# Performance work log

Hardware: AMD Instinct MI355X
Metric: run time of the kernel (lower is better)

## Reference

```python
import jax, jax.numpy as jnp
import numpy as np

B, C, D, H, K = 512, 112, 128, 8, 8  # batch, channels(=seq), d_model, heads, conv kernel
HD = D // H
SCALE = HD ** -0.5
BN_EPS = 1e-5
LN_EPS = 1e-5


def setup_inputs() -> dict:
    key = jax.random.key(0)
    ks = jax.random.split(key, 12)
    s = 0.05
    return {
        "x": jax.random.normal(ks[0], (B, C, D), jnp.float32),
        "conv_w": jax.random.normal(ks[1], (C, 1, K), jnp.float32) * s,
        "conv_b": jax.random.normal(ks[2], (C,), jnp.float32) * s,
        "bn_g": jnp.ones((C,), jnp.float32),
        "bn_b": jnp.zeros((C,), jnp.float32),
        "bn_m": jnp.zeros((C,), jnp.float32),
        "bn_v": jnp.ones((C,), jnp.float32),
        "wq": jax.random.normal(ks[3], (D, D), jnp.float32) * s,
        "bq": jax.random.normal(ks[4], (D,), jnp.float32) * s,
        "wk": jax.random.normal(ks[5], (D, D), jnp.float32) * s,
        "bk": jax.random.normal(ks[6], (D,), jnp.float32) * s,
        "wv": jax.random.normal(ks[7], (D, D), jnp.float32) * s,
        "bv": jax.random.normal(ks[8], (D,), jnp.float32) * s,
        "wo": jax.random.normal(ks[9], (D, D), jnp.float32) * s,
        "bo": jax.random.normal(ks[10], (D,), jnp.float32) * s,
        "ln_g": jnp.ones((D,), jnp.float32),
        "ln_b": jnp.zeros((D,), jnp.float32),
    }


def _forward(x, conv_w, conv_b, bn_g, bn_b, bn_m, bn_v,
             wq, bq, wk, bk, wv, bv, wo, bo, ln_g, ln_b):
    # resnet_1: depthwise Conv1d(padding='same', k=8) -> GELU -> BatchNorm1d (eval)
    # torch 'same' padding for even k: left = (k-1)//2 = 3, right = 4
    h = jax.lax.conv_general_dilated(
        x, conv_w, window_strides=(1,), padding=[(3, 4)],
        dimension_numbers=("NCH", "OIH", "NCH"), feature_group_count=C)
    h = h + conv_b[None, :, None]
    h = jax.nn.gelu(h, approximate=False)
    h = (h - bn_m[None, :, None]) * (bn_g[None, :, None] * jax.lax.rsqrt(bn_v + BN_EPS)[None, :, None]) + bn_b[None, :, None]
    src = x + h  # [B, C, D]; attention treats C as sequence dim

    # multi-head attention (hand-rolled, res_attention path with prev=None)
    q = (src @ wq.T + bq).reshape(B, C, H, HD).transpose(0, 2, 1, 3)  # [B,H,S,hd]
    k = (src @ wk.T + bk).reshape(B, C, H, HD).transpose(0, 2, 1, 3)
    v = (src @ wv.T + bv).reshape(B, C, H, HD).transpose(0, 2, 1, 3)
    scores = jnp.einsum("bhqd,bhkd->bhqk", q, k) * SCALE  # [B,H,S,S]
    attn = jax.nn.softmax(scores, axis=-1)
    out = jnp.einsum("bhqk,bhkd->bhqd", attn, v)  # [B,H,S,hd]
    out = out.transpose(0, 2, 1, 3).reshape(B, C, D)
    out = out @ wo.T + bo

    # residual + LayerNorm over last dim
    src = src + out
    mu = jnp.mean(src, axis=-1, keepdims=True)
    var = jnp.mean(jnp.square(src - mu), axis=-1, keepdims=True)
    src = (src - mu) * jax.lax.rsqrt(var + LN_EPS) * ln_g + ln_b
    return src


def reference(x, conv_w, conv_b, bn_g, bn_b, bn_m, bn_v,
              wq, bq, wk, bk, wv, bv, wo, bo, ln_g, ln_b):
    return _forward(x, conv_w, conv_b, bn_g, bn_b, bn_m, bn_v,
                    wq, bq, wk, bk, wv, bv, wo, bo, ln_g, ln_b)
```

## Files before the change

kernel.cpp:

```cpp
#include <hip/hip_runtime.h>
#include <hip/hip_bf16.h>

#define BB 512
#define CC 112
#define DD 128
#define HH 8
#define HD 16
#define KK 8
#define SROW 140
#define QS 1792

typedef unsigned short u16;
typedef short short8 __attribute__((ext_vector_type(8)));
typedef float f32x4 __attribute__((ext_vector_type(4)));
typedef float f32x16 __attribute__((ext_vector_type(16)));

#define MFMA16(a, b, c) __builtin_amdgcn_mfma_f32_16x16x32_bf16(a, b, c, 0, 0, 0)
#define MFMA32(a, b, c) __builtin_amdgcn_mfma_f32_32x32x16_bf16(a, b, c, 0, 0, 0)

__device__ inline u16 f2bf(float f) {
  union { float f; unsigned u; } v{f};
  unsigned r = (v.u + 0x7FFFu + ((v.u >> 16) & 1u)) >> 16;
  return (u16)r;
}
__device__ inline float bf2f(u16 u) {
  union { unsigned u; float f; } v;
  v.u = ((unsigned)u) << 16;
  return v.f;
}
__device__ inline unsigned pk2(float a, float b) {
  __hip_bfloat162 h = __float22bfloat162_rn(float2{a, b});
  union { __hip_bfloat162 h; unsigned u; } v{h};
  return v.u;
}

__device__ inline unsigned permx32(unsigned x) {
  unsigned a = x, b = x;
  asm("v_permlane32_swap_b32 %0, %1" : "+v"(a), "+v"(b));
  return (threadIdx.x & 32) ? a : b;
}
__device__ inline float permx32f(float x) {
  union { float f; unsigned u; } v{x};
  v.u = permx32(v.u);
  return v.f;
}

__global__ __launch_bounds__(256) void k_wcvt(
    const float* __restrict__ wq, const float* __restrict__ wk,
    const float* __restrict__ wv, const float* __restrict__ wo,
    u16* __restrict__ w_b) {
  const int i = (blockIdx.x * 256 + threadIdx.x);
  const int sel = i >> 12, off = i & 4095;
  const float* w = (sel == 0) ? wq : (sel == 1) ? wk : (sel == 2) ? wv : wo;
  const float4 v = ((const float4*)w)[off];
  ((uint2*)w_b)[i] = uint2{pk2(v.x, v.y), pk2(v.z, v.w)};
}

__global__ __launch_bounds__(1024, 4) void k_fused(
    const float* __restrict__ x, const float* __restrict__ cw,
    const float* __restrict__ cb, const float* __restrict__ bg,
    const float* __restrict__ bb_, const float* __restrict__ bm,
    const float* __restrict__ bv, const u16* __restrict__ w_b,
    const float* __restrict__ bq, const float* __restrict__ bk,
    const float* __restrict__ bvv, const float* __restrict__ bo,
    const float* __restrict__ lg, const float* __restrict__ lb,
    float* __restrict__ out) {
  __shared__ __attribute__((aligned(16))) u16 S[CC * SROW];
  __shared__ __attribute__((aligned(16))) u16 QL[HH * CC * HD];
  __shared__ __attribute__((aligned(16))) u16 KL[HH * CC * HD];
  __shared__ __attribute__((aligned(16))) u16 VTL[HH * HD * CC];
  const int b = blockIdx.x;
  const int t = threadIdx.x;
  const int wave = t >> 6, lane = t & 63;

  const int tg = t >> 3, s = t & 7;
  if (tg < CC) {
    const int row = tg, ch = tg;
    const float4 w0 = *(const float4*)(cw + ch * KK);
    const float4 w1 = *(const float4*)(cw + ch * KK + 4);
    const float cbv = cb[ch];
    const float bscale = bg[ch] * rsqrtf(bv[ch] + 1e-5f);
    const float bmv = bm[ch], bbv = bb_[ch];
    const float* __restrict__ xr = x + ((size_t)b * CC + row) * DD;
    float in[24];
#pragma unroll
    for (int f = 0; f < 6; ++f) {
      const int fi = 4 * s - 1 + f;
      float4 vv = {0.f, 0.f, 0.f, 0.f};
      if (fi >= 0 && fi < 32) vv = ((const float4*)xr)[fi];
      in[f * 4 + 0] = vv.x; in[f * 4 + 1] = vv.y;
      in[f * 4 + 2] = vv.z; in[f * 4 + 3] = vv.w;
    }
    unsigned pkv[8];
#pragma unroll
    for (int i2 = 0; i2 < 8; ++i2) {
      float oo[2];
#pragma unroll
      for (int j = 0; j < 2; ++j) {
        const int i = i2 * 2 + j;
        float a = 0.f;
        a = fmaf(in[i + 1], w0.x, a);
        a = fmaf(in[i + 2], w0.y, a);
        a = fmaf(in[i + 3], w0.z, a);
        a = fmaf(in[i + 4], w0.w, a);
        a = fmaf(in[i + 5], w1.x, a);
        a = fmaf(in[i + 6], w1.y, a);
        a = fmaf(in[i + 7], w1.z, a);
        a = fmaf(in[i + 8], w1.w, a);
        a += cbv;
        const float u = fmaf(0.044715f * a, a, 1.0f);
        const float e = __expf(a * u * -1.5957691216f);
        const float g = a * __frcp_rn(1.f + e);
        oo[j] = in[i + 4] + (g - bmv) * bscale + bbv;
      }
      pkv[i2] = pk2(oo[0], oo[1]);
    }
    u16* srow = S + row * SROW + s * 16;
#pragma unroll
    for (int k2 = 0; k2 < 4; ++k2)
      *(uint2*)(srow + k2 * 4) = ((uint2*)pkv)[k2];
  }
  __syncthreads();

  {
    const int h = wave >> 1, mh = wave & 1;
    const int quad = lane >> 4, n = lane & 15;
    short8 Bf0[4], Bf1[4], Bf2[4];
#pragma unroll
    for (int kf = 0; kf < 4; ++kf) {
      const int wi = (h * 16 + n) * DD + kf * 32 + quad * 8;
      Bf0[kf] = *(const short8*)(w_b + wi);
      Bf1[kf] = *(const short8*)(w_b + 16384 + wi);
      Bf2[kf] = *(const short8*)(w_b + 32768 + wi);
    }
    const float bqv = bq[h * 16 + n];
    const float bkv = bk[h * 16 + n];
    const float bvv2 = bvv[h * 16 + n];
    u16* qlh = QL + h * QS;
    u16* klh = KL + h * QS;
    u16* vlh = VTL + h * QS;
#pragma unroll
    for (int m = 0; m < 4; ++m) {
      const int mt = mh * 4 + m;
      if (mt < 7) {
        short8 A[4];
#pragma unroll
        for (int kf = 0; kf < 4; ++kf)
          A[kf] = *(const short8*)&S[(mt * 16 + n) * SROW + kf * 32 + quad * 8];
        f32x4 aq = {0.f, 0.f, 0.f, 0.f};
        f32x4 ak = {0.f, 0.f, 0.f, 0.f};
        f32x4 av = {0.f, 0.f, 0.f, 0.f};
#pragma unroll
        for (int kf = 0; kf < 4; ++kf) {
          aq = MFMA16(A[kf], Bf0[kf], aq);
          ak = MFMA16(A[kf], Bf1[kf], ak);
          av = MFMA16(A[kf], Bf2[kf], av);
        }
        const int row0 = mt * 16 + quad * 4;
#pragma unroll
        for (int r = 0; r < 4; ++r) {
          qlh[(row0 + r) * HD + n] = f2bf(aq[r] + bqv);
          klh[(row0 + r) * HD + n] = f2bf(ak[r] + bkv);
        }
        *(uint2*)&vlh[n * CC + row0] =
            uint2{pk2(av[0] + bvv2, av[1] + bvv2),
                  pk2(av[2] + bvv2, av[3] + bvv2)};
      }
    }
  }
  __syncthreads();

  {
    const int h = wave >> 1, qh = wave & 1;
    const int lo = lane & 31, hi = lane >> 5, hi8 = hi * 8;
    const u16* qlh = QL + h * QS;
    const u16* klh = KL + h * QS;
    const u16* vlh = VTL + h * QS;
    u16* aoh = QL + h * QS;
    for (int qi = 0; qi < 2; ++qi) {
      const int qt = qh * 2 + qi;
      const int qt0 = qt * 32;
      short8 Bq = {};
      if (qt0 + lo < CC) Bq = *(const short8*)(qlh + (qt0 + lo) * HD + hi8);
      f32x16 sa[4];
#pragma unroll
      for (int mt = 0; mt < 4; ++mt) {
        short8 Ak = {};
        const int key = mt * 32 + lo;
        if (key < CC) Ak = *(const short8*)(klh + key * HD + hi8);
        f32x16 z = {};
        sa[mt] = MFMA32(Ak, Bq, z);
      }
      const float C1 = 0.25f * 1.44269504088896341f;
      float mxp[4] = {-1e30f, -1e30f, -1e30f, -1e30f};
#pragma unroll
      for (int mt = 0; mt < 4; ++mt) {
        const int rmax = (mt == 3) ? 8 : 16;
#pragma unroll
        for (int r = 0; r < 16; ++r)
          if (r < rmax) mxp[r & 3] = fmaxf(mxp[r & 3], sa[mt][r]);
      }
      float mx = fmaxf(fmaxf(mxp[0], mxp[1]), fmaxf(mxp[2], mxp[3]));
      mx = fmaxf(mx, permx32f(mx));
      const float mxc = mx * C1;
      float sp[4] = {0.f, 0.f, 0.f, 0.f};
#pragma unroll
      for (int mt = 0; mt < 4; ++mt) {
        const int rmax = (mt == 3) ? 8 : 16;
#pragma unroll
        for (int r = 0; r < 16; ++r)
          if (r < rmax) {
            const float p = exp2f(fmaf(sa[mt][r], C1, -mxc));
            sa[mt][r] = p;
            sp[r & 3] += p;
          }
      }
      float sum = (sp[0] + sp[1]) + (sp[2] + sp[3]);
      sum += permx32f(sum);
      const float rinv = 1.f / sum;
      unsigned U0[4][4], U1[4][4];
#pragma unroll
      for (int mt = 0; mt < 4; ++mt) {
        const int rqmax = (mt == 3) ? 2 : 4;
#pragma unroll
        for (int rq = 0; rq < 4; ++rq)
          if (rq < rqmax) {
            U0[mt][rq] =
                pk2(sa[mt][4 * rq + 0] * rinv, sa[mt][4 * rq + 1] * rinv);
            U1[mt][rq] =
                pk2(sa[mt][4 * rq + 2] * rinv, sa[mt][4 * rq + 3] * rinv);
          }
      }
      f32x16 oacc = {};
#pragma unroll
      for (int kt = 0; kt < 7; ++kt) {
        const int mt = kt >> 1;
        const int c = 2 * (kt & 1);
        const unsigned own0 = hi ? U0[mt][c + 1] : U0[mt][c];
        const unsigned own1 = hi ? U1[mt][c + 1] : U1[mt][c];
        const unsigned snd0 = hi ? U0[mt][c] : U0[mt][c + 1];
        const unsigned snd1 = hi ? U1[mt][c] : U1[mt][c + 1];
        const unsigned got0 = permx32(snd0);
        const unsigned got1 = permx32(snd1);
        union { unsigned u[4]; short8 s; } ap;
        ap.u[0] = hi ? got0 : own0;
        ap.u[1] = hi ? got1 : own1;
        ap.u[2] = hi ? own0 : got0;
        ap.u[3] = hi ? own1 : got1;
        short8 Bv = {};
        if (lo < HD) Bv = *(const short8*)(vlh + lo * CC + kt * 16 + hi8);
        oacc = MFMA32(ap.s, Bv, oacc);
      }
      if (lo < HD) {
#pragma unroll
        for (int r = 0; r < 16; ++r) {
          const int rr = (r & 3) + 8 * (r >> 2) + 4 * hi;
          if (qt0 + rr < CC) aoh[(qt0 + rr) * HD + lo] = f2bf(oacc[r]);
        }
      }
    }
  }
  __syncthreads();

  if (wave < 7) {
    const int quad = lane >> 4, n = lane & 15;
    const int mt = wave;
    const u16* __restrict__ w_bo = w_b + 3 * 16384;
    short8 A[4];
#pragma unroll
    for (int kf = 0; kf < 4; ++kf) {
      const int head = 2 * kf + (quad >> 1);
      A[kf] = *(const short8*)&QL[head * QS + (mt * 16 + n) * HD + (quad & 1) * 8];
    }
    float v[8][4];
#pragma unroll
    for (int nt = 0; nt < 8; ++nt) {
      f32x4 acc = {0.f, 0.f, 0.f, 0.f};
#pragma unroll
      for (int kf = 0; kf < 4; ++kf) {
        const short8 Bf =
            *(const short8*)(w_bo + (nt * 16 + n) * DD + kf * 32 + quad * 8);
        acc = MFMA16(A[kf], Bf, acc);
      }
      const int col = nt * 16 + n;
      const float bcol = bo[col];
#pragma unroll
      for (int r = 0; r < 4; ++r)
        v[nt][r] = acc[r] + bcol +
                   bf2f(S[(mt * 16 + quad * 4 + r) * SROW + col]);
    }
    float sum[4] = {0.f, 0.f, 0.f, 0.f}, sq[4] = {0.f, 0.f, 0.f, 0.f};
#pragma unroll
    for (int nt = 0; nt < 8; ++nt)
#pragma unroll
      for (int r = 0; r < 4; ++r) {
        sum[r] += v[nt][r];
        sq[r] = fmaf(v[nt][r], v[nt][r], sq[r]);
      }
#pragma unroll
    for (int d = 1; d < 16; d <<= 1)
#pragma unroll
      for (int r = 0; r < 4; ++r) {
        sum[r] += __shfl_xor(sum[r], d);
        sq[r] += __shfl_xor(sq[r], d);
      }
    float mu[4], rs[4];
#pragma unroll
    for (int r = 0; r < 4; ++r) {
      mu[r] = sum[r] * (1.f / DD);
      const float var = sq[r] * (1.f / DD) - mu[r] * mu[r];
      rs[r] = rsqrtf(var + 1e-5f);
    }
#pragma unroll
    for (int nt = 0; nt < 8; ++nt) {
      const int col = nt * 16 + n;
      const float g = lg[col], be = lb[col];
#pragma unroll
      for (int r = 0; r < 4; ++r)
        out[((size_t)b * CC + mt * 16 + quad * 4 + r) * DD + col] =
            (v[nt][r] - mu[r]) * rs[r] * g + be;
    }
  }
}

extern "C" void kernel_launch(void* const* d_in, const int* in_sizes, int n_in,
                              void* d_out, int out_size, void* d_ws,
                              size_t ws_size, hipStream_t stream) {
  (void)in_sizes; (void)n_in; (void)out_size; (void)ws_size;
  const float* x   = (const float*)d_in[0];
  const float* cw  = (const float*)d_in[1];
  const float* cb  = (const float*)d_in[2];
  const float* bg  = (const float*)d_in[3];
  const float* bb  = (const float*)d_in[4];
  const float* bm  = (const float*)d_in[5];
  const float* bv  = (const float*)d_in[6];
  const float* wq  = (const float*)d_in[7];
  const float* bq  = (const float*)d_in[8];
  const float* wk  = (const float*)d_in[9];
  const float* bk  = (const float*)d_in[10];
  const float* wv  = (const float*)d_in[11];
  const float* bvv = (const float*)d_in[12];
  const float* wo  = (const float*)d_in[13];
  const float* bo  = (const float*)d_in[14];
  const float* lg  = (const float*)d_in[15];
  const float* lb  = (const float*)d_in[16];
  float* out = (float*)d_out;

  u16* w_b = (u16*)d_ws;

  k_wcvt<<<64, 256, 0, stream>>>(wq, wk, wv, wo, w_b);
  k_fused<<<BB, 1024, 0, stream>>>(x, cw, cb, bg, bb, bm, bv, w_b, bq, bk,
                                   bvv, bo, lg, lb, out);
}
```

Baseline: 173.3 us.

## Process two batches per block with software-pipelined phases and inline weight conversion

Each block now handles two batch elements and interleaves phases so the conv of the second batch overlaps the QKV/attention of the first, and the output projection of the first overlaps attention of the second. QKV projection and attention are merged into one phase, and V stays in registers and moves between lanes by shuffle instead of being stored to a transposed LDS buffer. The separate weight-conversion kernel is dropped; weights are read as fp32 and packed to bf16 inside the fused kernel. This removes a launch and some barriers, at the cost of redundant per-block weight conversion, more LDS per block (double buffers), only 256 blocks, and fewer resident blocks per CU since the occupancy hint was removed.

```diff
diff --git a/kernel.cpp b/kernel.cpp
--- a/kernel.cpp
+++ b/kernel.cpp
@@ -45,288 +45,313 @@
   return v.f;
 }
 
-__global__ __launch_bounds__(256) void k_wcvt(
+__device__ inline short8 ldw8(const float* __restrict__ p) {
+  const float4 a = *(const float4*)p;
+  const float4 c = *(const float4*)(p + 4);
+  union { unsigned u[4]; short8 s; } r;
+  r.u[0] = pk2(a.x, a.y);
+  r.u[1] = pk2(a.z, a.w);
+  r.u[2] = pk2(c.x, c.y);
+  r.u[3] = pk2(c.z, c.w);
+  return r.s;
+}
+
+__device__ __forceinline__ void conv_phase(
+    int b, u16* __restrict__ Sb, const float* __restrict__ x,
+    const float* __restrict__ cw, const float* __restrict__ cb,
+    const float* __restrict__ bg, const float* __restrict__ bb_,
+    const float* __restrict__ bm, const float* __restrict__ bv, int t) {
+  const int tg = t >> 3, s = t & 7;
+  if (tg >= CC) return;
+  const int row = tg, ch = tg;
+  const float4 w0 = *(const float4*)(cw + ch * KK);
+  const float4 w1 = *(const float4*)(cw + ch * KK + 4);
+  const float cbv = cb[ch];
+  const float bscale = bg[ch] * rsqrtf(bv[ch] + 1e-5f);
+  const float bmv = bm[ch], bbv = bb_[ch];
+  const float* __restrict__ xr = x + ((size_t)b * CC + row) * DD;
+  float in[24];
+#pragma unroll
+  for (int f = 0; f < 6; ++f) {
+    const int fi = 4 * s - 1 + f;
+    float4 vv = {0.f, 0.f, 0.f, 0.f};
+    if (fi >= 0 && fi < 32) vv = ((const float4*)xr)[fi];
+    in[f * 4 + 0] = vv.x; in[f * 4 + 1] = vv.y;
+    in[f * 4 + 2] = vv.z; in[f * 4 + 3] = vv.w;
+  }
+  unsigned pkv[8];
+#pragma unroll
+  for (int i2 = 0; i2 < 8; ++i2) {
+    float oo[2];
+#pragma unroll
+    for (int j = 0; j < 2; ++j) {
+      const int i = i2 * 2 + j;
+      float a = 0.f;
+      a = fmaf(in[i + 1], w0.x, a);
+      a = fmaf(in[i + 2], w0.y, a);
+      a = fmaf(in[i + 3], w0.z, a);
+      a = fmaf(in[i + 4], w0.w, a);
+      a = fmaf(in[i + 5], w1.x, a);
+      a = fmaf(in[i + 6], w1.y, a);
+      a = fmaf(in[i + 7], w1.z, a);
+      a = fmaf(in[i + 8], w1.w, a);
+      a += cbv;
+      const float u = fmaf(0.044715f * a, a, 1.0f);
+      const float e = __expf(a * u * -1.5957691216f);
+      const float g = a * __frcp_rn(1.f + e);
+      oo[j] = in[i + 4] + (g - bmv) * bscale + bbv;
+    }
+    pkv[i2] = pk2(oo[0], oo[1]);
+  }
+  u16* srow = Sb + row * SROW + s * 16;
+#pragma unroll
+  for (int k2 = 0; k2 < 4; ++k2)
+    *(uint2*)(srow + k2 * 4) = ((uint2*)pkv)[k2];
+}
+
+__device__ __forceinline__ void middle_phase(
+    const u16* __restrict__ Sb, u16* __restrict__ QOb, u16* __restrict__ KLb,
     const float* __restrict__ wq, const float* __restrict__ wk,
-    const float* __restrict__ wv, const float* __restrict__ wo,
-    u16* __restrict__ w_b) {
-  const int i = (blockIdx.x * 256 + threadIdx.x);
-  const int sel = i >> 12, off = i & 4095;
-  const float* w = (sel == 0) ? wq : (sel == 1) ? wk : (sel == 2) ? wv : wo;
-  const float4 v = ((const float4*)w)[off];
-  ((uint2*)w_b)[i] = uint2{pk2(v.x, v.y), pk2(v.z, v.w)};
-}
-
-__global__ __launch_bounds__(1024, 4) void k_fused(
+    const float* __restrict__ wv, const float* __restrict__ bq,
+    const float* __restrict__ bk, const float* __restrict__ bvv, int t) {
+  const int wave = t >> 6, lane = t & 63;
+  const int h = wave >> 1, qh = wave & 1;
+  const int quad = lane >> 4, n = lane & 15;
+  short8 Wq[4], Wk[4], Wv[4];
+#pragma unroll
+  for (int kf = 0; kf < 4; ++kf) {
+    const int off = (h * 16 + n) * DD + kf * 32 + quad * 8;
+    Wq[kf] = ldw8(wq + off);
+    Wk[kf] = ldw8(wk + off);
+    Wv[kf] = ldw8(wv + off);
+  }
+  const float bqv = bq[h * 16 + n];
+  const float bkv = bk[h * 16 + n];
+  const float bvv2 = bvv[h * 16 + n];
+  u16* qoh = QOb + h * QS;
+  u16* klh = KLb + h * QS;
+  unsigned pv[14];
+#pragma unroll
+  for (int mt = 0; mt < 7; ++mt) {
+    short8 A[4];
+#pragma unroll
+    for (int kf = 0; kf < 4; ++kf)
+      A[kf] = *(const short8*)&Sb[(mt * 16 + n) * SROW + kf * 32 + quad * 8];
+    f32x4 aq = {0.f, 0.f, 0.f, 0.f};
+    f32x4 ak = {0.f, 0.f, 0.f, 0.f};
+    f32x4 av = {0.f, 0.f, 0.f, 0.f};
+#pragma unroll
+    for (int kf = 0; kf < 4; ++kf) {
+      aq = MFMA16(A[kf], Wq[kf], aq);
+      ak = MFMA16(A[kf], Wk[kf], ak);
+      av = MFMA16(A[kf], Wv[kf], av);
+    }
+    const int row0 = mt * 16 + quad * 4;
+    const bool doq = qh ? (mt >= 4) : (mt < 4);
+    if (doq) {
+#pragma unroll
+      for (int r = 0; r < 4; ++r)
+        qoh[(row0 + r) * HD + n] = f2bf(aq[r] + bqv);
+    }
+#pragma unroll
+    for (int r = 0; r < 4; ++r)
+      klh[(row0 + r) * HD + n] = f2bf(ak[r] + bkv);
+    pv[2 * mt] = pk2(av[0] + bvv2, av[1] + bvv2);
+    pv[2 * mt + 1] = pk2(av[2] + bvv2, av[3] + bvv2);
+  }
+  unsigned pvp[14];
+#pragma unroll
+  for (int j = 0; j < 14; ++j) pvp[j] = __shfl_xor(pv[j], 16);
+
+  const int lo = lane & 31, hi = lane >> 5, hi8 = hi * 8;
+  for (int qi = 0; qi < 2; ++qi) {
+    const int qt = qh * 2 + qi;
+    const int qt0 = qt * 32;
+    short8 Bq = {};
+    if (qt0 + lo < CC) Bq = *(const short8*)(qoh + (qt0 + lo) * HD + hi8);
+    f32x16 sa[4];
+#pragma unroll
+    for (int mt = 0; mt < 4; ++mt) {
+      short8 Ak = {};
+      const int key = mt * 32 + lo;
+      if (key < CC) Ak = *(const short8*)(klh + key * HD + hi8);
+      f32x16 z = {};
+      sa[mt] = MFMA32(Ak, Bq, z);
+    }
+    const float C1 = 0.25f * 1.44269504088896341f;
+    float mxp[4] = {-1e30f, -1e30f, -1e30f, -1e30f};
+#pragma unroll
+    for (int mt = 0; mt < 4; ++mt) {
+      const int rmax = (mt == 3) ? 8 : 16;
+#pragma unroll
+      for (int r = 0; r < 16; ++r)
+        if (r < rmax) mxp[r & 3] = fmaxf(mxp[r & 3], sa[mt][r]);
+    }
+    float mx = fmaxf(fmaxf(mxp[0], mxp[1]), fmaxf(mxp[2], mxp[3]));
+    mx = fmaxf(mx, permx32f(mx));
+    const float mxc = mx * C1;
+    float sp[4] = {0.f, 0.f, 0.f, 0.f};
+#pragma unroll
+    for (int mt = 0; mt < 4; ++mt) {
+      const int rmax = (mt == 3) ? 8 : 16;
+#pragma unroll
+      for (int r = 0; r < 16; ++r)
+        if (r < rmax) {
+          const float p = exp2f(fmaf(sa[mt][r], C1, -mxc));
+          sa[mt][r] = p;
+          sp[r & 3] += p;
+        }
+    }
+    float sum = (sp[0] + sp[1]) + (sp[2] + sp[3]);
+    sum += permx32f(sum);
+    const float rinv = 1.f / sum;
+    unsigned U0[4][4], U1[4][4];
+#pragma unroll
+    for (int mt = 0; mt < 4; ++mt) {
+      const int rqmax = (mt == 3) ? 2 : 4;
+#pragma unroll
+      for (int rq = 0; rq < 4; ++rq)
+        if (rq < rqmax) {
+          U0[mt][rq] =
+              pk2(sa[mt][4 * rq + 0] * rinv, sa[mt][4 * rq + 1] * rinv);
+          U1[mt][rq] =
+              pk2(sa[mt][4 * rq + 2] * rinv, sa[mt][4 * rq + 3] * rinv);
+        }
+    }
+    f32x16 oacc = {};
+#pragma unroll
+    for (int kt = 0; kt < 7; ++kt) {
+      const int mt = kt >> 1;
+      const int c = 2 * (kt & 1);
+      const unsigned own0 = hi ? U0[mt][c + 1] : U0[mt][c];
+      const unsigned own1 = hi ? U1[mt][c + 1] : U1[mt][c];
+      const unsigned snd0 = hi ? U0[mt][c] : U0[mt][c + 1];
+      const unsigned snd1 = hi ? U1[mt][c] : U1[mt][c + 1];
+      const unsigned got0 = permx32(snd0);
+      const unsigned got1 = permx32(snd1);
+      union { unsigned u[4]; short8 s; } ap;
+      ap.u[0] = hi ? got0 : own0;
+      ap.u[1] = hi ? got1 : own1;
+      ap.u[2] = hi ? own0 : got0;
+      ap.u[3] = hi ? own1 : got1;
+      union { unsigned u[4]; short8 s; } bv;
+      bv.u[0] = pv[2 * kt];
+      bv.u[1] = pv[2 * kt + 1];
+      bv.u[2] = pvp[2 * kt];
+      bv.u[3] = pvp[2 * kt + 1];
+      oacc = MFMA32(ap.s, bv.s, oacc);
+    }
+    if (lo < HD) {
+#pragma unroll
+      for (int r = 0; r < 16; ++r) {
+        const int rr = (r & 3) + 8 * (r >> 2) + 4 * hi;
+        if (qt0 + rr < CC) qoh[(qt0 + rr) * HD + lo] = f2bf(oacc[r]);
+      }
+    }
+  }
+}
+
+__device__ __forceinline__ void out_phase(
+    int b, const u16* __restrict__ Sb, const u16* __restrict__ QOb,
+    const float* __restrict__ wo, const float* __restrict__ bo,
+    const float* __restrict__ lg, const float* __restrict__ lb,
+    float* __restrict__ out, int t) {
+  const int wave = t >> 6, lane = t & 63;
+  const int quad = lane >> 4, n = lane & 15;
+  const int mt = wave;
+  short8 A[4];
+#pragma unroll
+  for (int kf = 0; kf < 4; ++kf) {
+    const int head = 2 * kf + (quad >> 1);
+    A[kf] =
+        *(const short8*)&QOb[head * QS + (mt * 16 + n) * HD + (quad & 1) * 8];
+  }
+  float v[8][4];
+#pragma unroll
+  for (int nt = 0; nt < 8; ++nt) {
+    f32x4 acc = {0.f, 0.f, 0.f, 0.f};
+#pragma unroll
+    for (int kf = 0; kf < 4; ++kf) {
+      const short8 Bf = ldw8(wo + (nt * 16 + n) * DD + kf * 32 + quad * 8);
+      acc = MFMA16(A[kf], Bf, acc);
+    }
+    const int col = nt * 16 + n;
+    const float bcol = bo[col];
+#pragma unroll
+    for (int r = 0; r < 4; ++r)
+      v[nt][r] =
+          acc[r] + bcol + bf2f(Sb[(mt * 16 + quad * 4 + r) * SROW + col]);
+  }
+  float sum[4] = {0.f, 0.f, 0.f, 0.f}, sq[4] = {0.f, 0.f, 0.f, 0.f};
+#pragma unroll
+  for (int nt = 0; nt < 8; ++nt)
+#pragma unroll
+    for (int r = 0; r < 4; ++r) {
+      sum[r] += v[nt][r];
+      sq[r] = fmaf(v[nt][r], v[nt][r], sq[r]);
+    }
+#pragma unroll
+  for (int d = 1; d < 16; d <<= 1)
+#pragma unroll
+    for (int r = 0; r < 4; ++r) {
+      sum[r] += __shfl_xor(sum[r], d);
+      sq[r] += __shfl_xor(sq[r], d);
+    }
+  float mu[4], rs[4];
+#pragma unroll
+  for (int r = 0; r < 4; ++r) {
+    mu[r] = sum[r] * (1.f / DD);
+    const float var = sq[r] * (1.f / DD) - mu[r] * mu[r];
+    rs[r] = rsqrtf(var + 1e-5f);
+  }
+#pragma unroll
+  for (int nt = 0; nt < 8; ++nt) {
+    const int col = nt * 16 + n;
+    const float g = lg[col], be = lb[col];
+#pragma unroll
+    for (int r = 0; r < 4; ++r)
+      out[((size_t)b * CC + mt * 16 + quad * 4 + r) * DD + col] =
+          (v[nt][r] - mu[r]) * rs[r] * g + be;
+  }
+}
+
+__global__ __launch_bounds__(1024) void k_fused2(
     const float* __restrict__ x, const float* __restrict__ cw,
     const float* __restrict__ cb, const float* __restrict__ bg,
     const float* __restrict__ bb_, const float* __restrict__ bm,
-    const float* __restrict__ bv, const u16* __restrict__ w_b,
-    const float* __restrict__ bq, const float* __restrict__ bk,
-    const float* __restrict__ bvv, const float* __restrict__ bo,
-    const float* __restrict__ lg, const float* __restrict__ lb,
-    float* __restrict__ out) {
-  __shared__ __attribute__((aligned(16))) u16 S[CC * SROW];
-  __shared__ __attribute__((aligned(16))) u16 QL[HH * CC * HD];
+    const float* __restrict__ bv, const float* __restrict__ wq,
+    const float* __restrict__ bq, const float* __restrict__ wk,
+    const float* __restrict__ bk, const float* __restrict__ wv,
+    const float* __restrict__ bvv, const float* __restrict__ wo,
+    const float* __restrict__ bo, const float* __restrict__ lg,
+    const float* __restrict__ lb, float* __restrict__ out) {
+  __shared__ __attribute__((aligned(16))) u16 S0[CC * SROW];
+  __shared__ __attribute__((aligned(16))) u16 S1[CC * SROW];
+  __shared__ __attribute__((aligned(16))) u16 QO0[HH * CC * HD];
+  __shared__ __attribute__((aligned(16))) u16 QO1[HH * CC * HD];
   __shared__ __attribute__((aligned(16))) u16 KL[HH * CC * HD];
-  __shared__ __attribute__((aligned(16))) u16 VTL[HH * HD * CC];
-  const int b = blockIdx.x;
   const int t = threadIdx.x;
-  const int wave = t >> 6, lane = t & 63;
-
-  const int tg = t >> 3, s = t & 7;
-  if (tg < CC) {
-    const int row = tg, ch = tg;
-    const float4 w0 = *(const float4*)(cw + ch * KK);
-    const float4 w1 = *(const float4*)(cw + ch * KK + 4);
-    const float cbv = cb[ch];
-    const float bscale = bg[ch] * rsqrtf(bv[ch] + 1e-5f);
-    const float bmv = bm[ch], bbv = bb_[ch];
-    const float* __restrict__ xr = x + ((size_t)b * CC + row) * DD;
-    float in[24];
-#pragma unroll
-    for (int f = 0; f < 6; ++f) {
-      const int fi = 4 * s - 1 + f;
-      float4 vv = {0.f, 0.f, 0.f, 0.f};
-      if (fi >= 0 && fi < 32) vv = ((const float4*)xr)[fi];
-      in[f * 4 + 0] = vv.x; in[f * 4 + 1] = vv.y;
-      in[f * 4 + 2] = vv.z; in[f * 4 + 3] = vv.w;
-    }
-    unsigned pkv[8];
-#pragma unroll
-    for (int i2 = 0; i2 < 8; ++i2) {
-      float oo[2];
-#pragma unroll
-      for (int j = 0; j < 2; ++j) {
-        const int i = i2 * 2 + j;
-        float a = 0.f;
-        a = fmaf(in[i + 1], w0.x, a);
-        a = fmaf(in[i + 2], w0.y, a);
-        a = fmaf(in[i + 3], w0.z, a);
-        a = fmaf(in[i + 4], w0.w, a);
-        a = fmaf(in[i + 5], w1.x, a);
-        a = fmaf(in[i + 6], w1.y, a);
-        a = fmaf(in[i + 7], w1.z, a);
-        a = fmaf(in[i + 8], w1.w, a);
-        a += cbv;
-        const float u = fmaf(0.044715f * a, a, 1.0f);
-        const float e = __expf(a * u * -1.5957691216f);
-        const float g = a * __frcp_rn(1.f + e);
-        oo[j] = in[i + 4] + (g - bmv) * bscale + bbv;
-      }
-      pkv[i2] = pk2(oo[0], oo[1]);
-    }
-    u16* srow = S + row * SROW + s * 16;
-#pragma unroll
-    for (int k2 = 0; k2 < 4; ++k2)
-      *(uint2*)(srow + k2 * 4) = ((uint2*)pkv)[k2];
-  }
+  const int wave = t >> 6;
+  const int b0 = blockIdx.x * 2, b1 = b0 + 1;
+
+  conv_phase(b0, S0, x, cw, cb, bg, bb_, bm, bv, t);
   __syncthreads();
 
-  {
-    const int h = wave >> 1, mh = wave & 1;
-    const int quad = lane >> 4, n = lane & 15;
-    short8 Bf0[4], Bf1[4], Bf2[4];
-#pragma unroll
-    for (int kf = 0; kf < 4; ++kf) {
-      const int wi = (h * 16 + n) * DD + kf * 32 + quad * 8;
-      Bf0[kf] = *(const short8*)(w_b + wi);
-      Bf1[kf] = *(const short8*)(w_b + 16384 + wi);
-      Bf2[kf] = *(const short8*)(w_b + 32768 + wi);
-    }
-    const float bqv = bq[h * 16 + n];
-    const float bkv = bk[h * 16 + n];
-    const float bvv2 = bvv[h * 16 + n];
-    u16* qlh = QL + h * QS;
-    u16* klh = KL + h * QS;
-    u16* vlh = VTL + h * QS;
-#pragma unroll
-    for (int m = 0; m < 4; ++m) {
-      const int mt = mh * 4 + m;
-      if (mt < 7) {
-        short8 A[4];
-#pragma unroll
-        for (int kf = 0; kf < 4; ++kf)
-          A[kf] = *(const short8*)&S[(mt * 16 + n) * SROW + kf * 32 + quad * 8];
-        f32x4 aq = {0.f, 0.f, 0.f, 0.f};
-        f32x4 ak = {0.f, 0.f, 0.f, 0.f};
-        f32x4 av = {0.f, 0.f, 0.f, 0.f};
-#pragma unroll
-        for (int kf = 0; kf < 4; ++kf) {
-          aq = MFMA16(A[kf], Bf0[kf], aq);
-          ak = MFMA16(A[kf], Bf1[kf], ak);
-          av = MFMA16(A[kf], Bf2[kf], av);
-        }
-        const int row0 = mt * 16 + quad * 4;
-#pragma unroll
-        for (int r = 0; r < 4; ++r) {
-          qlh[(row0 + r) * HD + n] = f2bf(aq[r] + bqv);
-          klh[(row0 + r) * HD + n] = f2bf(ak[r] + bkv);
-        }
-        *(uint2*)&vlh[n * CC + row0] =
-            uint2{pk2(av[0] + bvv2, av[1] + bvv2),
-                  pk2(av[2] + bvv2, av[3] + bvv2)};
-      }
-    }
-  }
+  middle_phase(S0, QO0, KL, wq, wk, wv, bq, bk, bvv, t);
+  conv_phase(b1, S1, x, cw, cb, bg, bb_, bm, bv, t);
   __syncthreads();
 
-  {
-    const int h = wave >> 1, qh = wave & 1;
-    const int lo = lane & 31, hi = lane >> 5, hi8 = hi * 8;
-    const u16* qlh = QL + h * QS;
-    const u16* klh = KL + h * QS;
-    const u16* vlh = VTL + h * QS;
-    u16* aoh = QL + h * QS;
-    for (int qi = 0; qi < 2; ++qi) {
-      const int qt = qh * 2 + qi;
-      const int qt0 = qt * 32;
-      short8 Bq = {};
-      if (qt0 + lo < CC) Bq = *(const short8*)(qlh + (qt0 + lo) * HD + hi8);
-      f32x16 sa[4];
-#pragma unroll
-      for (int mt = 0; mt < 4; ++mt) {
-        short8 Ak = {};
-        const int key = mt * 32 + lo;
-        if (key < CC) Ak = *(const short8*)(klh + key * HD + hi8);
-        f32x16 z = {};
-        sa[mt] = MFMA32(Ak, Bq, z);
-      }
-      const float C1 = 0.25f * 1.44269504088896341f;
-      float mxp[4] = {-1e30f, -1e30f, -1e30f, -1e30f};
-#pragma unroll
-      for (int mt = 0; mt < 4; ++mt) {
-        const int rmax = (mt == 3) ? 8 : 16;
-#pragma unroll
-        for (int r = 0; r < 16; ++r)
-          if (r < rmax) mxp[r & 3] = fmaxf(mxp[r & 3], sa[mt][r]);
-      }
-      float mx = fmaxf(fmaxf(mxp[0], mxp[1]), fmaxf(mxp[2], mxp[3]));
-      mx = fmaxf(mx, permx32f(mx));
-      const float mxc = mx * C1;
-      float sp[4] = {0.f, 0.f, 0.f, 0.f};
-#pragma unroll
-      for (int mt = 0; mt < 4; ++mt) {
-        const int rmax = (mt == 3) ? 8 : 16;
-#pragma unroll
-        for (int r = 0; r < 16; ++r)
-          if (r < rmax) {
-            const float p = exp2f(fmaf(sa[mt][r], C1, -mxc));
-            sa[mt][r] = p;
-            sp[r & 3] += p;
-          }
-      }
-      float sum = (sp[0] + sp[1]) + (sp[2] + sp[3]);
-      sum += permx32f(sum);
-      const float rinv = 1.f / sum;
-      unsigned U0[4][4], U1[4][4];
-#pragma unroll
-      for (int mt = 0; mt < 4; ++mt) {
-        const int rqmax = (mt == 3) ? 2 : 4;
-#pragma unroll
-        for (int rq = 0; rq < 4; ++rq)
-          if (rq < rqmax) {
-            U0[mt][rq] =
-                pk2(sa[mt][4 * rq + 0] * rinv, sa[mt][4 * rq + 1] * rinv);
-            U1[mt][rq] =
-                pk2(sa[mt][4 * rq + 2] * rinv, sa[mt][4 * rq + 3] * rinv);
-          }
-      }
-      f32x16 oacc = {};
-#pragma unroll
-      for (int kt = 0; kt < 7; ++kt) {
-        const int mt = kt >> 1;
-        const int c = 2 * (kt & 1);
-        const unsigned own0 = hi ? U0[mt][c + 1] : U0[mt][c];
-        const unsigned own1 = hi ? U1[mt][c + 1] : U1[mt][c];
-        const unsigned snd0 = hi ? U0[mt][c] : U0[mt][c + 1];
-        const unsigned snd1 = hi ? U1[mt][c] : U1[mt][c + 1];
-        const unsigned got0 = permx32(snd0);
-        const unsigned got1 = permx32(snd1);
-        union { unsigned u[4]; short8 s; } ap;
-        ap.u[0] = hi ? got0 : own0;
-        ap.u[1] = hi ? got1 : own1;
-        ap.u[2] = hi ? own0 : got0;
-        ap.u[3] = hi ? own1 : got1;
-        short8 Bv = {};
-        if (lo < HD) Bv = *(const short8*)(vlh + lo * CC + kt * 16 + hi8);
-        oacc = MFMA32(ap.s, Bv, oacc);
-      }
-      if (lo < HD) {
-#pragma unroll
-        for (int r = 0; r < 16; ++r) {
-          const int rr = (r & 3) + 8 * (r >> 2) + 4 * hi;
-          if (qt0 + rr < CC) aoh[(qt0 + rr) * HD + lo] = f2bf(oacc[r]);
-        }
-      }
-    }
-  }
+  if (wave < 7) out_phase(b0, S0, QO0, wo, bo, lg, lb, out, t);
+  middle_phase(S1, QO1, KL, wq, wk, wv, bq, bk, bvv, t);
   __syncthreads();
 
-  if (wave < 7) {
-    const int quad = lane >> 4, n = lane & 15;
-    const int mt = wave;
-    const u16* __restrict__ w_bo = w_b + 3 * 16384;
-    short8 A[4];
-#pragma unroll
-    for (int kf = 0; kf < 4; ++kf) {
-      const int head = 2 * kf + (quad >> 1);
-      A[kf] = *(const short8*)&QL[head * QS + (mt * 16 + n) * HD + (quad & 1) * 8];
-    }
-    float v[8][4];
-#pragma unroll
-    for (int nt = 0; nt < 8; ++nt) {
-      f32x4 acc = {0.f, 0.f, 0.f, 0.f};
-#pragma unroll
-      for (int kf = 0; kf < 4; ++kf) {
-        const short8 Bf =
-            *(const short8*)(w_bo + (nt * 16 + n) * DD + kf * 32 + quad * 8);
-        acc = MFMA16(A[kf], Bf, acc);
-      }
-      const int col = nt * 16 + n;
-      const float bcol = bo[col];
-#pragma unroll
-      for (int r = 0; r < 4; ++r)
-        v[nt][r] = acc[r] + bcol +
-                   bf2f(S[(mt * 16 + quad * 4 + r) * SROW + col]);
-    }
-    float sum[4] = {0.f, 0.f, 0.f, 0.f}, sq[4] = {0.f, 0.f, 0.f, 0.f};
-#pragma unroll
-    for (int nt = 0; nt < 8; ++nt)
-#pragma unroll
-      for (int r = 0; r < 4; ++r) {
-        sum[r] += v[nt][r];
-        sq[r] = fmaf(v[nt][r], v[nt][r], sq[r]);
-      }
-#pragma unroll
-    for (int d = 1; d < 16; d <<= 1)
-#pragma unroll
-      for (int r = 0; r < 4; ++r) {
-        sum[r] += __shfl_xor(sum[r], d);
-        sq[r] += __shfl_xor(sq[r], d);
-      }
-    float mu[4], rs[4];
-#pragma unroll
-    for (int r = 0; r < 4; ++r) {
-      mu[r] = sum[r] * (1.f / DD);
-      const float var = sq[r] * (1.f / DD) - mu[r] * mu[r];
-      rs[r] = rsqrtf(var + 1e-5f);
-    }
-#pragma unroll
-    for (int nt = 0; nt < 8; ++nt) {
-      const int col = nt * 16 + n;
-      const float g = lg[col], be = lb[col];
-#pragma unroll
-      for (int r = 0; r < 4; ++r)
-        out[((size_t)b * CC + mt * 16 + quad * 4 + r) * DD + col] =
-            (v[nt][r] - mu[r]) * rs[r] * g + be;
-    }
-  }
+  if (wave < 7) out_phase(b1, S1, QO1, wo, bo, lg, lb, out, t);
 }
 
 extern "C" void kernel_launch(void* const* d_in, const int* in_sizes, int n_in,
                               void* d_out, int out_size, void* d_ws,
                               size_t ws_size, hipStream_t stream) {
-  (void)in_sizes; (void)n_in; (void)out_size; (void)ws_size;
+  (void)in_sizes; (void)n_in; (void)out_size; (void)d_ws; (void)ws_size;
   const float* x   = (const float*)d_in[0];
   const float* cw  = (const float*)d_in[1];
   const float* cb  = (const float*)d_in[2];
@@ -346,9 +371,6 @@
   const float* lb  = (const float*)d_in[16];
   float* out = (float*)d_out;
 
-  u16* w_b = (u16*)d_ws;
-
-  k_wcvt<<<64, 256, 0, stream>>>(wq, wk, wv, wo, w_b);
-  k_fused<<<BB, 1024, 0, stream>>>(x, cw, cb, bg, bb, bm, bv, w_b, bq, bk,
-                                   bvv, bo, lg, lb, out);
-}
+  k_fused2<<<BB / 2, 1024, 0, stream>>>(x, cw, cb, bg, bb, bm, bv, wq, bq,
+                                        wk, bk, wv, bvv, wo, bo, lg, lb, out);
+}
```

Measured after the change: 198.1 us. +14.3%, slower.

## Split fused kernel into head-group attention blocks and separate output-projection kernel

Applied to the files above, without the earlier changes.

The single 1024-thread fused kernel becomes two kernels. The first launches two 512-thread blocks per batch, each handling four heads: both recompute the conv/GELU/BN prologue, and one of them writes src to global memory as bf16. Each block writes its attention output as bf16 to a global buffer, so the QKV shared-memory buffers are halved. A second kernel then does the output projection, residual add and LayerNorm from those global buffers. The goal is more blocks and occupancy per CU, at the cost of duplicated prologue work, an extra launch and global round-trips for src and the attention output.

```diff
diff --git a/kernel.cpp b/kernel.cpp
--- a/kernel.cpp
+++ b/kernel.cpp
@@ -8,7 +8,7 @@
 #define HD 16
 #define KK 8
 #define SROW 140
-#define QS 1792
+#define QSL 1792
 
 typedef unsigned short u16;
 typedef short short8 __attribute__((ext_vector_type(8)));
@@ -56,24 +56,25 @@
   ((uint2*)w_b)[i] = uint2{pk2(v.x, v.y), pk2(v.z, v.w)};
 }
 
-__global__ __launch_bounds__(1024, 4) void k_fused(
+__global__ __launch_bounds__(512, 4) void k_attn4(
     const float* __restrict__ x, const float* __restrict__ cw,
     const float* __restrict__ cb, const float* __restrict__ bg,
     const float* __restrict__ bb_, const float* __restrict__ bm,
     const float* __restrict__ bv, const u16* __restrict__ w_b,
     const float* __restrict__ bq, const float* __restrict__ bk,
-    const float* __restrict__ bvv, const float* __restrict__ bo,
-    const float* __restrict__ lg, const float* __restrict__ lb,
-    float* __restrict__ out) {
+    const float* __restrict__ bvv,
+    u16* __restrict__ src_b, u16* __restrict__ ob) {
   __shared__ __attribute__((aligned(16))) u16 S[CC * SROW];
-  __shared__ __attribute__((aligned(16))) u16 QL[HH * CC * HD];
-  __shared__ __attribute__((aligned(16))) u16 KL[HH * CC * HD];
-  __shared__ __attribute__((aligned(16))) u16 VTL[HH * HD * CC];
-  const int b = blockIdx.x;
+  __shared__ __attribute__((aligned(16))) u16 QL[4 * CC * HD];
+  __shared__ __attribute__((aligned(16))) u16 KL[4 * CC * HD];
+  __shared__ __attribute__((aligned(16))) u16 VTL[4 * CC * HD];
+  const int bid = blockIdx.x;
+  const int b = bid & (BB - 1);
+  const int g = bid >> 9;
   const int t = threadIdx.x;
   const int wave = t >> 6, lane = t & 63;
 
-  const int tg = t >> 3, s = t & 7;
+  const int tg = t >> 2, sub = t & 3;
   if (tg < CC) {
     const int row = tg, ch = tg;
     const float4 w0 = *(const float4*)(cw + ch * KK);
@@ -82,18 +83,18 @@
     const float bscale = bg[ch] * rsqrtf(bv[ch] + 1e-5f);
     const float bmv = bm[ch], bbv = bb_[ch];
     const float* __restrict__ xr = x + ((size_t)b * CC + row) * DD;
-    float in[24];
-#pragma unroll
-    for (int f = 0; f < 6; ++f) {
-      const int fi = 4 * s - 1 + f;
+    float in[40];
+#pragma unroll
+    for (int f = 0; f < 10; ++f) {
+      const int fi = 8 * sub - 1 + f;
       float4 vv = {0.f, 0.f, 0.f, 0.f};
       if (fi >= 0 && fi < 32) vv = ((const float4*)xr)[fi];
       in[f * 4 + 0] = vv.x; in[f * 4 + 1] = vv.y;
       in[f * 4 + 2] = vv.z; in[f * 4 + 3] = vv.w;
     }
-    unsigned pkv[8];
-#pragma unroll
-    for (int i2 = 0; i2 < 8; ++i2) {
+    unsigned pkv[16];
+#pragma unroll
+    for (int i2 = 0; i2 < 16; ++i2) {
       float oo[2];
 #pragma unroll
       for (int j = 0; j < 2; ++j) {
@@ -110,20 +111,26 @@
         a += cbv;
         const float u = fmaf(0.044715f * a, a, 1.0f);
         const float e = __expf(a * u * -1.5957691216f);
-        const float g = a * __frcp_rn(1.f + e);
-        oo[j] = in[i + 4] + (g - bmv) * bscale + bbv;
+        const float g2 = a * __frcp_rn(1.f + e);
+        oo[j] = in[i + 4] + (g2 - bmv) * bscale + bbv;
       }
       pkv[i2] = pk2(oo[0], oo[1]);
     }
-    u16* srow = S + row * SROW + s * 16;
-#pragma unroll
-    for (int k2 = 0; k2 < 4; ++k2)
+    u16* srow = S + row * SROW + sub * 32;
+#pragma unroll
+    for (int k2 = 0; k2 < 8; ++k2)
       *(uint2*)(srow + k2 * 4) = ((uint2*)pkv)[k2];
+    if (g == 0) {
+      uint4* gsr = (uint4*)(src_b + ((size_t)b * CC + row) * DD + sub * 32);
+#pragma unroll
+      for (int k4 = 0; k4 < 4; ++k4) gsr[k4] = ((uint4*)pkv)[k4];
+    }
   }
   __syncthreads();
 
   {
-    const int h = wave >> 1, mh = wave & 1;
+    const int h_local = wave >> 1, mh = wave & 1;
+    const int h = g * 4 + h_local;
     const int quad = lane >> 4, n = lane & 15;
     short8 Bf0[4], Bf1[4], Bf2[4];
 #pragma unroll
@@ -136,9 +143,9 @@
     const float bqv = bq[h * 16 + n];
     const float bkv = bk[h * 16 + n];
     const float bvv2 = bvv[h * 16 + n];
-    u16* qlh = QL + h * QS;
-    u16* klh = KL + h * QS;
-    u16* vlh = VTL + h * QS;
+    u16* qlh = QL + h_local * QSL;
+    u16* klh = KL + h_local * QSL;
+    u16* vlh = VTL + h_local * QSL;
 #pragma unroll
     for (int m = 0; m < 4; ++m) {
       const int mt = mh * 4 + m;
@@ -171,12 +178,12 @@
   __syncthreads();
 
   {
-    const int h = wave >> 1, qh = wave & 1;
+    const int h_local = wave >> 1, qh = wave & 1;
+    const int h = g * 4 + h_local;
     const int lo = lane & 31, hi = lane >> 5, hi8 = hi * 8;
-    const u16* qlh = QL + h * QS;
-    const u16* klh = KL + h * QS;
-    const u16* vlh = VTL + h * QS;
-    u16* aoh = QL + h * QS;
+    const u16* qlh = QL + h_local * QSL;
+    const u16* klh = KL + h_local * QSL;
+    const u16* vlh = VTL + h_local * QSL;
     for (int qi = 0; qi < 2; ++qi) {
       const int qt = qh * 2 + qi;
       const int qt0 = qt * 32;
@@ -255,71 +262,78 @@
 #pragma unroll
         for (int r = 0; r < 16; ++r) {
           const int rr = (r & 3) + 8 * (r >> 2) + 4 * hi;
-          if (qt0 + rr < CC) aoh[(qt0 + rr) * HD + lo] = f2bf(oacc[r]);
+          if (qt0 + rr < CC)
+            ob[((size_t)b * CC + qt0 + rr) * DD + h * HD + lo] =
+                f2bf(oacc[r]);
         }
       }
     }
   }
-  __syncthreads();
-
-  if (wave < 7) {
-    const int quad = lane >> 4, n = lane & 15;
-    const int mt = wave;
-    const u16* __restrict__ w_bo = w_b + 3 * 16384;
-    short8 A[4];
+}
+
+__global__ __launch_bounds__(448, 4) void k_out(
+    const u16* __restrict__ ob, const u16* __restrict__ w_bo,
+    const float* __restrict__ bo, const u16* __restrict__ src_b,
+    const float* __restrict__ lg, const float* __restrict__ lb,
+    float* __restrict__ out) {
+  const int b = blockIdx.x;
+  const int t = threadIdx.x;
+  const int wave = t >> 6, lane = t & 63;
+  const int quad = lane >> 4, n = lane & 15;
+  const int mt = wave;
+  short8 A[4];
+#pragma unroll
+  for (int kf = 0; kf < 4; ++kf)
+    A[kf] = *(const short8*)(ob + ((size_t)b * CC + mt * 16 + n) * DD +
+                             kf * 32 + quad * 8);
+  float v[8][4];
+#pragma unroll
+  for (int nt = 0; nt < 8; ++nt) {
+    f32x4 acc = {0.f, 0.f, 0.f, 0.f};
 #pragma unroll
     for (int kf = 0; kf < 4; ++kf) {
-      const int head = 2 * kf + (quad >> 1);
-      A[kf] = *(const short8*)&QL[head * QS + (mt * 16 + n) * HD + (quad & 1) * 8];
-    }
-    float v[8][4];
-#pragma unroll
-    for (int nt = 0; nt < 8; ++nt) {
-      f32x4 acc = {0.f, 0.f, 0.f, 0.f};
-#pragma unroll
-      for (int kf = 0; kf < 4; ++kf) {
-        const short8 Bf =
-            *(const short8*)(w_bo + (nt * 16 + n) * DD + kf * 32 + quad * 8);
-        acc = MFMA16(A[kf], Bf, acc);
-      }
-      const int col = nt * 16 + n;
-      const float bcol = bo[col];
-#pragma unroll
-      for (int r = 0; r < 4; ++r)
-        v[nt][r] = acc[r] + bcol +
-                   bf2f(S[(mt * 16 + quad * 4 + r) * SROW + col]);
-    }
-    float sum[4] = {0.f, 0.f, 0.f, 0.f}, sq[4] = {0.f, 0.f, 0.f, 0.f};
-#pragma unroll
-    for (int nt = 0; nt < 8; ++nt)
-#pragma unroll
-      for (int r = 0; r < 4; ++r) {
-        sum[r] += v[nt][r];
-        sq[r] = fmaf(v[nt][r], v[nt][r], sq[r]);
-      }
-#pragma unroll
-    for (int d = 1; d < 16; d <<= 1)
-#pragma unroll
-      for (int r = 0; r < 4; ++r) {
-        sum[r] += __shfl_xor(sum[r], d);
-        sq[r] += __shfl_xor(sq[r], d);
-      }
-    float mu[4], rs[4];
+      const short8 Bf =
+          *(const short8*)(w_bo + (nt * 16 + n) * DD + kf * 32 + quad * 8);
+      acc = MFMA16(A[kf], Bf, acc);
+    }
+    const int col = nt * 16 + n;
+    const float bcol = bo[col];
+#pragma unroll
+    for (int r = 0; r < 4; ++r)
+      v[nt][r] =
+          acc[r] + bcol +
+          bf2f(src_b[((size_t)b * CC + mt * 16 + quad * 4 + r) * DD + col]);
+  }
+  float sum[4] = {0.f, 0.f, 0.f, 0.f}, sq[4] = {0.f, 0.f, 0.f, 0.f};
+#pragma unroll
+  for (int nt = 0; nt < 8; ++nt)
 #pragma unroll
     for (int r = 0; r < 4; ++r) {
-      mu[r] = sum[r] * (1.f / DD);
-      const float var = sq[r] * (1.f / DD) - mu[r] * mu[r];
-      rs[r] = rsqrtf(var + 1e-5f);
-    }
-#pragma unroll
-    for (int nt = 0; nt < 8; ++nt) {
-      const int col = nt * 16 + n;
-      const float g = lg[col], be = lb[col];
-#pragma unroll
-      for (int r = 0; r < 4; ++r)
-        out[((size_t)b * CC + mt * 16 + quad * 4 + r) * DD + col] =
-            (v[nt][r] - mu[r]) * rs[r] * g + be;
-    }
+      sum[r] += v[nt][r];
+      sq[r] = fmaf(v[nt][r], v[nt][r], sq[r]);
+    }
+#pragma unroll
+  for (int d = 1; d < 16; d <<= 1)
+#pragma unroll
+    for (int r = 0; r < 4; ++r) {
+      sum[r] += __shfl_xor(sum[r], d);
+      sq[r] += __shfl_xor(sq[r], d);
+    }
+  float mu[4], rs[4];
+#pragma unroll
+  for (int r = 0; r < 4; ++r) {
+    mu[r] = sum[r] * (1.f / DD);
+    const float var = sq[r] * (1.f / DD) - mu[r] * mu[r];
+    rs[r] = rsqrtf(var + 1e-5f);
+  }
+#pragma unroll
+  for (int nt = 0; nt < 8; ++nt) {
+    const int col = nt * 16 + n;
+    const float g = lg[col], be = lb[col];
+#pragma unroll
+    for (int r = 0; r < 4; ++r)
+      out[((size_t)b * CC + mt * 16 + quad * 4 + r) * DD + col] =
+          (v[nt][r] - mu[r]) * rs[r] * g + be;
   }
 }
 
@@ -346,9 +360,14 @@
   const float* lb  = (const float*)d_in[16];
   float* out = (float*)d_out;
 
-  u16* w_b = (u16*)d_ws;
+  const size_t NE = (size_t)BB * CC * DD;
+  u16* ub = (u16*)d_ws;
+  u16* src_b = ub;
+  u16* o_b   = ub + NE;
+  u16* w_b   = ub + 2 * NE;
 
   k_wcvt<<<64, 256, 0, stream>>>(wq, wk, wv, wo, w_b);
-  k_fused<<<BB, 1024, 0, stream>>>(x, cw, cb, bg, bb, bm, bv, w_b, bq, bk,
-                                   bvv, bo, lg, lb, out);
-}
+  k_attn4<<<2 * BB, 512, 0, stream>>>(x, cw, cb, bg, bb, bm, bv, w_b, bq, bk,
+                                      bvv, src_b, o_b);
+  k_out<<<BB, 448, 0, stream>>>(o_b, w_b + 3 * 16384, bo, src_b, lg, lb, out);
+}
```

Result: slower. 177.2 us (+2.3%).
